# Optimization experiments

Measured on AMD Instinct MI355X. Metric: run time of the kernel, lower is better.

Reference implementation:

```python
import jax, jax.numpy as jnp
import numpy as np

N, L, D, H, DFF = 16, 192, 512, 8, 2048
HD = D // H


def _mha(q, k, v, wq, bq, wk, bk, wv, bv, wo, bo, mask=None):
    # q: [B, Lq, D], k/v: [B, Lk, D]
    B, Lq, _ = q.shape
    def proj(x, W, b):
        y = x @ W + b
        return y.reshape(B, -1, H, HD).transpose(0, 2, 1, 3)  # [B, H, L, HD]
    Q, K, V = proj(q, wq, bq), proj(k, wk, bk), proj(v, wv, bv)
    QK = jnp.einsum('bhqd,bhkd->bhqk', Q, K) / jnp.sqrt(jnp.asarray(HD, Q.dtype))
    if mask is not None:
        QK = QK + (1.0 - mask) * (-1e9)
    A = jax.nn.softmax(QK, axis=-1)
    out = jnp.einsum('bhqk,bhkd->bhqd', A, V).transpose(0, 2, 1, 3).reshape(B, Lq, D)
    return out @ wo + bo


def _ln(x, g, b, eps=1e-6):
    mu = x.mean(-1, keepdims=True)
    var = ((x - mu) ** 2).mean(-1, keepdims=True)
    return (x - mu) / jnp.sqrt(var + eps) * g + b


def setup_inputs() -> dict:
    key = jax.random.key(0)
    ks = jax.random.split(key, 16)
    w = lambda k, sh: jax.random.normal(k, sh, jnp.float32) * 0.02
    inp = {
        'S': jax.random.normal(ks[0], (N, L, D), jnp.float32),
        'padding_mask': jax.random.randint(ks[1], (N * N, 1, 1, L), 0, 2, dtype=jnp.int32),
        'training': 0,
    }
    for i, nm in enumerate(['ca_wq', 'ca_wk', 'ca_wv', 'ca_wo', 'ia_wq', 'ia_wk', 'ia_wv', 'ia_wo']):
        inp[nm] = w(ks[2 + i], (D, D))
        inp[nm.replace('w', 'b')] = jnp.zeros((D,), jnp.float32)
    inp['ffn_w1'] = w(ks[10], (D, DFF)); inp['ffn_b1'] = jnp.zeros((DFF,), jnp.float32)
    inp['ffn_w2'] = w(ks[11], (DFF, D)); inp['ffn_b2'] = jnp.zeros((D,), jnp.float32)
    inp['ln1_g'] = jnp.ones((D,), jnp.float32); inp['ln1_b'] = jnp.zeros((D,), jnp.float32)
    inp['ln2_g'] = jnp.ones((D,), jnp.float32); inp['ln2_b'] = jnp.zeros((D,), jnp.float32)
    return inp


def reference(S, ca_wq, ca_bq, ca_wk, ca_bk, ca_wv, ca_bv, ca_wo, ca_bo,
              ia_wq, ia_bq, ia_wk, ia_bk, ia_wv, ia_bv, ia_wo, ia_bo,
              ffn_w1, ffn_b1, ffn_w2, ffn_b2, ln1_g, ln1_b, ln2_g, ln2_b,
              padding_mask, training):
    # training == 0 -> dropout layers are identity (inference mode)
    mask = padding_mask.astype(S.dtype)
    n, l, d = S.shape
    # all-pairs cross attention: query seq i attends to key/value seq j
    queries = jnp.repeat(S, n, axis=0)   # [n*n, l, d]
    keyvalue = jnp.tile(S, (n, 1, 1))    # [n*n, l, d]
    S_attn = _mha(queries, keyvalue, keyvalue,
                  ca_wq, ca_bq, ca_wk, ca_bk, ca_wv, ca_bv, ca_wo, ca_bo, mask=mask)
    S_attn = S_attn.reshape(n, n, l, d).transpose(1, 2, 0, 3).reshape(n * l, n, d)
    S_flip = S.reshape(n * l, 1, d)
    S_attn = _mha(S_flip, S_attn, S_attn,
                  ia_wq, ia_bq, ia_wk, ia_bk, ia_wv, ia_bv, ia_wo, ia_bo)
    S_attn = S_attn.reshape(n, l, d)
    S_norm = _ln(S + S_attn, ln1_g, ln1_b)
    S_ffn = jax.nn.relu(S_norm @ ffn_w1 + ffn_b1) @ ffn_w2 + ffn_b2
    return _ln(S_norm + S_ffn, ln2_g, ln2_b)
```

## Files before the change

### kernel.cpp

```cpp
#include <hip/hip_runtime.h>


using u16 = unsigned short;
using u32 = unsigned int;
typedef __attribute__((ext_vector_type(8))) short short8;
typedef __attribute__((ext_vector_type(4))) float f32x4;

__device__ __forceinline__ u32 cvtpk(float lo, float hi) {
  u32 r;
  asm("v_cvt_pk_bf16_f32 %0, %1, %2" : "=v"(r) : "v"(lo), "v"(hi));
  return r;
}
__device__ __forceinline__ u16 f2bf(float f) { return (u16)cvtpk(f, f); }
__device__ __forceinline__ float bf2f(u16 h) {
  return __uint_as_float(((u32)h) << 16);
}
__device__ __forceinline__ f32x4 mfma16(short8 a, short8 b, f32x4 c) {
  return __builtin_amdgcn_mfma_f32_16x16x32_bf16(a, b, c, 0, 0, 0);
}
__device__ __forceinline__ void gload16(const void* g, u16* l) {
  __builtin_amdgcn_global_load_lds(
      (const __attribute__((address_space(1))) void*)g,
      (__attribute__((address_space(3))) void*)l, 16, 0, 0);
}

template<int ROWS, int NT>
__device__ __forceinline__ void stage_g16(u16* lds, const u16* __restrict__ src,
                                          int ld, int tid) {
  constexpr int UNITS = ROWS * 8;
  constexpr int WV = NT / 64;
  int lane = tid & 63, w = tid >> 6;
  #pragma unroll
  for (int u = 0; u < UNITS / NT; ++u) {
    int base = (u * WV + w) * 64;
    int unit = base + lane;
    int row = unit >> 3, co = unit & 7;
    gload16(src + (long)row * ld + ((co ^ (row & 7)) << 3), lds + base * 8);
  }
}
template<int ROWS, int NT>
__device__ __forceinline__ void stage_f32(u16* lds, const float* __restrict__ src,
                                          int ld, int tid) {
  constexpr int UNITS = ROWS * 8;
  #pragma unroll
  for (int u = 0; u < UNITS / NT; ++u) {
    int unit = tid + u * NT;
    int row = unit >> 3, co = unit & 7;
    const float* g = src + (long)row * ld + (co << 3);
    float4 a = *(const float4*)g;
    float4 b = *(const float4*)(g + 4);
    u32 p[4] = {cvtpk(a.x, a.y), cvtpk(a.z, a.w),
                cvtpk(b.x, b.y), cvtpk(b.z, b.w)};
    *(uint4*)&lds[(row << 6) + ((co ^ (row & 7)) << 3)] = *(const uint4*)p;
  }
}

template<typename AT, typename BT, int BM, int BN, int WM, int WN>
__device__ __forceinline__ void gemm_core(const AT* __restrict__ A, int lda,
                                          const BT* __restrict__ Bt, int ldb, int K,
                                          u16* As, u16* Bs,
                                          f32x4 (&acc)[BM / (WM * 16)][BN / (WN * 16)]) {
  constexpr int NT = WM * WN * 64;
  constexpr int MI = BM / (WM * 16), NJ = BN / (WN * 16);
  int tid = threadIdx.x, lane = tid & 63, wid = tid >> 6;
  int wr = wid % WM, wc = wid / WM;
  int g = lane >> 4, c = lane & 15;
  #pragma unroll
  for (int mi = 0; mi < MI; ++mi)
    #pragma unroll
    for (int nj = 0; nj < NJ; ++nj)
      acc[mi][nj] = f32x4{0.f, 0.f, 0.f, 0.f};
  for (int kb = 0; kb < K; kb += 64) {
    __syncthreads();
    if constexpr (sizeof(AT) == 4) stage_f32<BM, NT>(As, A + kb, lda, tid);
    else                           stage_g16<BM, NT>(As, A + kb, lda, tid);
    if constexpr (sizeof(BT) == 4) stage_f32<BN, NT>(Bs, Bt + kb, ldb, tid);
    else                           stage_g16<BN, NT>(Bs, Bt + kb, ldb, tid);
    __syncthreads();
    #pragma unroll
    for (int kk = 0; kk < 2; ++kk) {
      int sl = ((kk * 4 + g) ^ (c & 7)) << 3;
      short8 af[MI], bfr[NJ];
      #pragma unroll
      for (int mi = 0; mi < MI; ++mi)
        af[mi] = *(const short8*)&As[((wr * (BM / WM) + mi * 16 + c) << 6) + sl];
      #pragma unroll
      for (int nj = 0; nj < NJ; ++nj)
        bfr[nj] = *(const short8*)&Bs[((wc * (BN / WN) + nj * 16 + c) << 6) + sl];
      #pragma unroll
      for (int mi = 0; mi < MI; ++mi)
        #pragma unroll
        for (int nj = 0; nj < NJ; ++nj)
          acc[mi][nj] = mfma16(af[mi], bfr[nj], acc[mi][nj]);
    }
  }
}

__global__ __launch_bounds__(256) void k_cast(const float* __restrict__ S,
                                              u16* __restrict__ Sb) {
  int idx = (blockIdx.x * 256 + threadIdx.x) * 8;
  float4 a = *(const float4*)(S + idx);
  float4 b = *(const float4*)(S + idx + 4);
  u32 p[4] = {cvtpk(a.x, a.y), cvtpk(a.z, a.w),
              cvtpk(b.x, b.y), cvtpk(b.z, b.w)};
  *(uint4*)(Sb + idx) = *(const uint4*)p;
}

struct TJob { const float* src; u16* dst; int R, C, tile0; };
struct TJobs { TJob j[9]; };

__global__ __launch_bounds__(256) void k_transpose(TJobs jobs) {
  __shared__ float tile[32][33];
  int t = blockIdx.x;
  int ji = 0;
  #pragma unroll
  for (int k = 1; k < 9; ++k)
    if (t >= jobs.j[k].tile0) ji = k;
  TJob jb = jobs.j[ji];
  int lt = t - jb.tile0;
  int tpr = jb.C >> 5;
  int tr = lt / tpr, tc = lt % tpr;
  int tid = threadIdx.x;
  #pragma unroll
  for (int u = 0; u < 4; ++u) {
    int e = tid + u * 256;
    int r = e >> 5, cc = e & 31;
    tile[r][cc] = jb.src[(long)(tr * 32 + r) * jb.C + tc * 32 + cc];
  }
  __syncthreads();
  #pragma unroll
  for (int u = 0; u < 4; ++u) {
    int e = tid + u * 256;
    int r = e >> 5, cc = e & 31;
    jb.dst[(long)(tc * 32 + r) * jb.R + tr * 32 + cc] = f2bf(tile[cc][r]);
  }
}

__global__ __launch_bounds__(256) void k_qkv(const u16* __restrict__ Sb,
    const u16* __restrict__ btAll,
    const float* __restrict__ b0, const float* __restrict__ b1,
    const float* __restrict__ b2, const float* __restrict__ b3,
    u16* __restrict__ Qc, u16* __restrict__ Kc, u16* __restrict__ Vt,
    u16* __restrict__ Qi) {
  __shared__ u16 SH[16384];
  int f = blockIdx.x;
  int swz = (f & 7) * 48 + (f >> 3);
  int mb = swz >> 4, nb = swz & 15;
  f32x4 acc[4][4];
  gemm_core<u16, u16, 128, 128, 2, 2>(Sb + (long)mb * 128 * 512, 512,
                                      btAll + (long)nb * 128 * 512, 512, 512,
                                      SH, SH + 8192, acc);
  int z = nb >> 2;
  const float* bias = z == 0 ? b0 : z == 1 ? b1 : z == 2 ? b2 : b3;
  float scale = (z == 0 || z == 3) ? 0.125f : 1.0f;
  int lane = threadIdx.x & 63, wid = threadIdx.x >> 6;
  int wr = wid & 1, wc = wid >> 1, g = lane >> 4, cl = lane & 15;
  #pragma unroll
  for (int mi = 0; mi < 4; ++mi)
    #pragma unroll
    for (int nj = 0; nj < 4; ++nj)
      #pragma unroll
      for (int r = 0; r < 4; ++r) {
        int row = mb * 128 + wr * 64 + mi * 16 + g * 4 + r;
        int cz = (nb & 3) * 128 + wc * 64 + nj * 16 + cl;
        float v = (acc[mi][nj][r] + bias[cz]) * scale;
        int seq = row / 192, t = row % 192, h = cz >> 6, hd = cz & 63;
        if (z == 0)      Qc[((long)(seq * 8 + h) * 192 + t) * 64 + hd] = f2bf(v);
        else if (z == 1) Kc[((long)(seq * 8 + h) * 192 + t) * 64 + hd] = f2bf(v);
        else if (z == 2) Vt[((long)(seq * 8 + h) * 64 + hd) * 192 + t] = f2bf(v);
        else             Qi[(long)row * 512 + cz] = f2bf(v);
      }
}

__global__ __launch_bounds__(256) void k_attn_up(const u16* __restrict__ Qc,
    const u16* __restrict__ Kc, const u16* __restrict__ VtG,
    const int* __restrict__ mask, u16* __restrict__ AC,
    const u16* __restrict__ Qi, const float* __restrict__ wk,
    u16* __restrict__ U, int attnBlocks) {
  __shared__ __align__(16) u16 SH[24960];
  int bid = blockIdx.x;
  int tid = threadIdx.x, lane = tid & 63, w = tid >> 6;
  int g = lane >> 4, c = lane & 15;
  if (bid < attnBlocks) {
    u16* Ks = SH;
    u16* Vs = SH + 12288;
    float* mbf = (float*)(SH + 24576);
    int b = bid >> 3, h = bid & 7;
    int i = b >> 4, j = b & 15;
    int qb = w * 48;

    const u16* Kbase = Kc + (long)(j * 8 + h) * 192 * 64;
    #pragma unroll
    for (int u = 0; u < 6; ++u) {
      int base = (u * 4 + w) * 64;
      int unit = base + lane;
      int row = unit >> 3, co = unit & 7;
      gload16(Kbase + (long)row * 64 + ((co ^ (row & 7)) << 3), Ks + base * 8);
    }
    const u16* Vbase = VtG + (long)(j * 8 + h) * 64 * 192;
    #pragma unroll
    for (int u = 0; u < 6; ++u) {
      int base = (u * 4 + w) * 64;
      int unit = base + lane;
      int row = unit / 24, co = unit - row * 24;
      gload16(Vbase + (long)row * 192 + ((co ^ (row & 7)) << 3), Vs + base * 8);
    }
    short8 bq[3][2];
    const u16* Qbase = Qc + (long)(i * 8 + h) * 192 * 64;
    #pragma unroll
    for (int nj = 0; nj < 3; ++nj)
      #pragma unroll
      for (int ks = 0; ks < 2; ++ks)
        bq[nj][ks] = *(const short8*)(Qbase + (long)(qb + nj * 16 + c) * 64 + ks * 32 + g * 8);
    if (tid < 192) mbf[tid] = mask[(long)b * 192 + tid] ? 0.f : -1e9f;
    __syncthreads();

    f32x4 oa[4][3];
    #pragma unroll
    for (int mi = 0; mi < 4; ++mi)
      #pragma unroll
      for (int nj = 0; nj < 3; ++nj)
        oa[mi][nj] = f32x4{0.f, 0.f, 0.f, 0.f};
    float sm[3] = {0.f, 0.f, 0.f};
    int srcLo = c | ((g & 1) << 5);
    int srcHi = srcLo + 16;
    int hi = g & 2;

    #pragma unroll 2
    for (int s = 0; s < 6; ++s) {
      short8 ak[2][2];
      #pragma unroll
      for (int kh = 0; kh < 2; ++kh) {
        int row = (2 * s + kh) * 16 + c;
        #pragma unroll
        for (int ks = 0; ks < 2; ++ks)
          ak[kh][ks] = *(const short8*)&Ks[(row << 6) + (((ks * 4 + g) ^ (c & 7)) << 3)];
      }
      f32x4 sa[2][3];
      __builtin_amdgcn_s_setprio(1);
      #pragma unroll
      for (int kh = 0; kh < 2; ++kh)
        #pragma unroll
        for (int nj = 0; nj < 3; ++nj) {
          sa[kh][nj] = mfma16(ak[kh][0], bq[nj][0], f32x4{0.f, 0.f, 0.f, 0.f});
          sa[kh][nj] = mfma16(ak[kh][1], bq[nj][1], sa[kh][nj]);
        }
      __builtin_amdgcn_s_setprio(0);
      u32 pk[2][3][2];
      #pragma unroll
      for (int kh = 0; kh < 2; ++kh) {
        f32x4 m4 = *(const f32x4*)&mbf[(2 * s + kh) * 16 + g * 4];
        #pragma unroll
        for (int nj = 0; nj < 3; ++nj) {
          float p0 = __expf(sa[kh][nj][0] + m4[0]);
          float p1 = __expf(sa[kh][nj][1] + m4[1]);
          float p2 = __expf(sa[kh][nj][2] + m4[2]);
          float p3 = __expf(sa[kh][nj][3] + m4[3]);
          sm[nj] += (p0 + p1) + (p2 + p3);
          pk[kh][nj][0] = cvtpk(p0, p1);
          pk[kh][nj][1] = cvtpk(p2, p3);
        }
      }
      short8 bfg[3];
      #pragma unroll
      for (int nj = 0; nj < 3; ++nj) {
        u32 w0a = (u32)__shfl((int)pk[0][nj][0], srcLo);
        u32 w0b = (u32)__shfl((int)pk[1][nj][0], srcLo);
        u32 w1a = (u32)__shfl((int)pk[0][nj][1], srcLo);
        u32 w1b = (u32)__shfl((int)pk[1][nj][1], srcLo);
        u32 w2a = (u32)__shfl((int)pk[0][nj][0], srcHi);
        u32 w2b = (u32)__shfl((int)pk[1][nj][0], srcHi);
        u32 w3a = (u32)__shfl((int)pk[0][nj][1], srcHi);
        u32 w3b = (u32)__shfl((int)pk[1][nj][1], srcHi);
        union { u32 u[4]; short8 s8; } bf;
        bf.u[0] = hi ? w0b : w0a;
        bf.u[1] = hi ? w1b : w1a;
        bf.u[2] = hi ? w2b : w2a;
        bf.u[3] = hi ? w3b : w3a;
        bfg[nj] = bf.s8;
      }
      int sl = ((s * 4 + g) ^ (c & 7)) << 3;
      __builtin_amdgcn_s_setprio(1);
      #pragma unroll
      for (int mi = 0; mi < 4; ++mi) {
        short8 av = *(const short8*)&Vs[(mi * 16 + c) * 192 + sl];
        #pragma unroll
        for (int nj = 0; nj < 3; ++nj)
          oa[mi][nj] = mfma16(av, bfg[nj], oa[mi][nj]);
      }
      __builtin_amdgcn_s_setprio(0);
    }
    #pragma unroll
    for (int nj = 0; nj < 3; ++nj) {
      sm[nj] += __shfl_xor(sm[nj], 16);
      sm[nj] += __shfl_xor(sm[nj], 32);
    }
    #pragma unroll
    for (int nj = 0; nj < 3; ++nj) {
      float rs = 1.0f / sm[nj];
      int q = qb + nj * 16 + c;
      u16* dst = AC + ((long)(b * 192 + q)) * 512 + h * 64 + g * 4;
      #pragma unroll
      for (int mi = 0; mi < 4; ++mi) {
        u32 p2[2] = {cvtpk(oa[mi][nj][0] * rs, oa[mi][nj][1] * rs),
                     cvtpk(oa[mi][nj][2] * rs, oa[mi][nj][3] * rs)};
        *(uint2*)(dst + mi * 16) = *(const uint2*)p2;
      }
    }
  } else {
    u16* As = SH;
    u16* Bs = SH + 8192;
    int t = bid - attnBlocks;
    int mb = t % 24, r2 = t / 24;
    int nb = r2 & 3, h = r2 >> 2;
    f32x4 acc[4][4];
    gemm_core<u16, float, 128, 128, 2, 2>(Qi + (long)mb * 128 * 512 + h * 64, 512,
                                          wk + (long)nb * 128 * 512 + h * 64, 512, 64,
                                          As, Bs, acc);
    int wr = w & 1, wc = w >> 1, cl = lane & 15;
    #pragma unroll
    for (int mi = 0; mi < 4; ++mi)
      #pragma unroll
      for (int nj = 0; nj < 4; ++nj)
        #pragma unroll
        for (int r = 0; r < 4; ++r) {
          int row = mb * 128 + wr * 64 + mi * 16 + g * 4 + r;
          int col = nb * 128 + wc * 64 + nj * 16 + cl;
          U[((long)row * 8 + h) * 512 + col] = f2bf(acc[mi][nj][r]);
        }
  }
}

__global__ __launch_bounds__(512, 1) void k_oproj8(const u16* __restrict__ AC,
    const u16* __restrict__ woT, const float* __restrict__ bo,
    u16* __restrict__ S2) {
  extern __shared__ u16 LDS[];
  int f = blockIdx.x;
  int swz = (f & 7) * 48 + (f >> 3);
  int mb = swz >> 1, nb = swz & 1;
  int tid = threadIdx.x, lane = tid & 63, wid = tid >> 6;
  int wr = wid >> 2, wc = wid & 3;
  int g = lane >> 4, c = lane & 15;
  const u16* Abase = AC + (long)mb * 256 * 512;
  const u16* Bbase = woT + (long)nb * 256 * 512;

  auto STAGE = [&](int opOff, int buf, int half, int kt, const u16* base) {
    u16* ldst = LDS + opOff + buf * 16384 + half * 8192;
    const u16* gsrc = base + (long)half * 128 * 512 + kt * 64;
    #pragma unroll
    for (int u = 0; u < 2; ++u) {
      int unit = tid + u * 512;
      int row = unit >> 3, co = unit & 7;
      gload16(gsrc + (long)row * 512 + ((co ^ (row & 7)) << 3), ldst + unit * 8);
    }
  };

  f32x4 acc[8][4];
  #pragma unroll
  for (int mi = 0; mi < 8; ++mi)
    #pragma unroll
    for (int nj = 0; nj < 4; ++nj)
      acc[mi][nj] = f32x4{0.f, 0.f, 0.f, 0.f};

  STAGE(0, 0, 0, 0, Abase);     STAGE(0, 0, 1, 0, Abase);
  STAGE(32768, 0, 0, 0, Bbase); STAGE(32768, 0, 1, 0, Bbase);
  STAGE(0, 1, 0, 1, Abase);     STAGE(0, 1, 1, 1, Abase);
  STAGE(32768, 1, 0, 1, Bbase); STAGE(32768, 1, 1, 1, Bbase);
  asm volatile("s_waitcnt vmcnt(8)");
  __builtin_amdgcn_s_barrier();

  short8 aLo[8], aHi[8], bLo[4], bHi[4];
  for (int t = 0; t < 8; ++t) {
    int buf = t & 1;
    int abase = buf * 16384, bbase = 32768 + buf * 16384;
    #pragma unroll
    for (int m = 0; m < 4; ++m)
      #pragma unroll
      for (int kk = 0; kk < 2; ++kk)
        aLo[m * 2 + kk] = *(const short8*)&LDS[abase +
            (wr * 128 + m * 16 + c) * 64 + (((kk * 4 + g) ^ (c & 7)) << 3)];
    #pragma unroll
    for (int n = 0; n < 2; ++n)
      #pragma unroll
      for (int kk = 0; kk < 2; ++kk)
        bLo[n * 2 + kk] = *(const short8*)&LDS[bbase +
            (wc * 64 + n * 16 + c) * 64 + (((kk * 4 + g) ^ (c & 7)) << 3)];
    __builtin_amdgcn_s_barrier();
    asm volatile("s_waitcnt lgkmcnt(0)");
    __builtin_amdgcn_sched_barrier(0);
    __builtin_amdgcn_s_setprio(1);
    #pragma unroll
    for (int m = 0; m < 4; ++m)
      #pragma unroll
      for (int n = 0; n < 2; ++n)
        #pragma unroll
        for (int kk = 0; kk < 2; ++kk)
          acc[m][n] = mfma16(aLo[m * 2 + kk], bLo[n * 2 + kk], acc[m][n]);
    __builtin_amdgcn_s_setprio(0);
    __builtin_amdgcn_s_barrier();
    #pragma unroll
    for (int m = 0; m < 4; ++m)
      #pragma unroll
      for (int kk = 0; kk < 2; ++kk)
        aHi[m * 2 + kk] = *(const short8*)&LDS[abase +
            (wr * 128 + (4 + m) * 16 + c) * 64 + (((kk * 4 + g) ^ (c & 7)) << 3)];
    __builtin_amdgcn_s_barrier();
    asm volatile("s_waitcnt lgkmcnt(0)");
    __builtin_amdgcn_sched_barrier(0);
    __builtin_amdgcn_s_setprio(1);
    #pragma unroll
    for (int m = 0; m < 4; ++m)
      #pragma unroll
      for (int n = 0; n < 2; ++n)
        #pragma unroll
        for (int kk = 0; kk < 2; ++kk)
          acc[4 + m][n] = mfma16(aHi[m * 2 + kk], bLo[n * 2 + kk], acc[4 + m][n]);
    __builtin_amdgcn_s_setprio(0);
    __builtin_amdgcn_s_barrier();
    #pragma unroll
    for (int n = 0; n < 2; ++n)
      #pragma unroll
      for (int kk = 0; kk < 2; ++kk)
        bHi[n * 2 + kk] = *(const short8*)&LDS[bbase +
            (wc * 64 + (2 + n) * 16 + c) * 64 + (((kk * 4 + g) ^ (c & 7)) << 3)];
    if (t < 6) {
      STAGE(0, buf, 0, t + 2, Abase);
      STAGE(0, buf, 1, t + 2, Abase);
    }
    __builtin_amdgcn_s_barrier();
    asm volatile("s_waitcnt lgkmcnt(0)");
    __builtin_amdgcn_sched_barrier(0);
    __builtin_amdgcn_s_setprio(1);
    #pragma unroll
    for (int m = 0; m < 4; ++m)
      #pragma unroll
      for (int n = 0; n < 2; ++n)
        #pragma unroll
        for (int kk = 0; kk < 2; ++kk)
          acc[m][2 + n] = mfma16(aLo[m * 2 + kk], bHi[n * 2 + kk], acc[m][2 + n]);
    __builtin_amdgcn_s_setprio(0);
    __builtin_amdgcn_s_barrier();
    if (t < 6) {
      STAGE(32768, buf, 0, t + 2, Bbase);
      STAGE(32768, buf, 1, t + 2, Bbase);
    }
    __builtin_amdgcn_s_setprio(1);
    #pragma unroll
    for (int m = 0; m < 4; ++m)
      #pragma unroll
      for (int n = 0; n < 2; ++n)
        #pragma unroll
        for (int kk = 0; kk < 2; ++kk)
          acc[4 + m][2 + n] = mfma16(aHi[m * 2 + kk], bHi[n * 2 + kk], acc[4 + m][2 + n]);
    __builtin_amdgcn_s_setprio(0);
    if (t < 6)      asm volatile("s_waitcnt vmcnt(8)");
    else if (t == 6) asm volatile("s_waitcnt vmcnt(0)");
    if (t < 7) __builtin_amdgcn_s_barrier();
  }
  #pragma unroll
  for (int nj = 0; nj < 4; ++nj) {
    int col = nb * 256 + wc * 64 + nj * 16 + c;
    float bv = bo[col];
    #pragma unroll
    for (int mi = 0; mi < 8; ++mi)
      #pragma unroll
      for (int r = 0; r < 4; ++r) {
        int row = mb * 256 + wr * 128 + mi * 16 + g * 4 + r;
        S2[(long)row * 512 + col] = f2bf(acc[mi][nj][r] + bv);
      }
  }
}

__global__ __launch_bounds__(256) void k_ia_attn(const u16* __restrict__ S2,
    const u16* __restrict__ U, const u16* __restrict__ Qi,
    const float* __restrict__ bk, u16* __restrict__ Y) {
  __shared__ u16 s2[16 * 520];
  __shared__ float Lp[4][16][17];
  __shared__ float aL[8][16];
  __shared__ float cL[8];
  int tok = blockIdx.x;
  int tid = threadIdx.x, lane = tid & 63, w = tid >> 6;
  {
    const u16* src = S2 + (long)tok * 512;
    #pragma unroll
    for (int u = 0; u < 4; ++u) {
      int e = tid + u * 256;
      int r = e >> 6, cc = (e & 63) << 3;
      *(uint4*)&s2[r * 520 + cc] = *(const uint4*)(src + (long)r * 3072 * 512 + cc);
    }
  }
  if (w == 0) {
    int h = lane >> 3, p = lane & 7;
    short8 qv = *(const short8*)(Qi + (long)tok * 512 + h * 64 + p * 8);
    const float* bkp = bk + h * 64 + p * 8;
    float s = 0.f;
    #pragma unroll
    for (int v = 0; v < 8; ++v) s += bf2f((u16)qv[v]) * bkp[v];
    s += __shfl_xor(s, 1); s += __shfl_xor(s, 2); s += __shfl_xor(s, 4);
    if (p == 0) cL[h] = s;
  }
  __syncthreads();
  {
    int g = lane >> 4, c = lane & 15;
    const u16* Ub = U + (long)tok * 4096 + (long)(c & 7) * 512;
    f32x4 accL = {0.f, 0.f, 0.f, 0.f};
    #pragma unroll
    for (int kk = 0; kk < 4; ++kk) {
      int d = w * 128 + kk * 32 + g * 8;
      short8 aS = *(const short8*)&s2[c * 520 + d];
      short8 bU = *(const short8*)(Ub + d);
      accL = mfma16(aS, bU, accL);
    }
    #pragma unroll
    for (int r = 0; r < 4; ++r) Lp[w][g * 4 + r][c] = accL[r];
  }
  __syncthreads();
  if (w == 0) {
    int h = lane & 7, i0 = lane >> 3;
    float L0 = Lp[0][i0][h] + Lp[1][i0][h] + Lp[2][i0][h] + Lp[3][i0][h] + cL[h];
    float L1 = Lp[0][i0 + 8][h] + Lp[1][i0 + 8][h] + Lp[2][i0 + 8][h] +
               Lp[3][i0 + 8][h] + cL[h];
    float e0 = __expf(L0), e1 = __expf(L1);
    float s = e0 + e1;
    s += __shfl_xor(s, 8); s += __shfl_xor(s, 16); s += __shfl_xor(s, 32);
    float rs = 1.0f / s;
    aL[h][i0] = e0 * rs;
    aL[h][i0 + 8] = e1 * rs;
  }
  __syncthreads();
  {
    int h = tid & 7, d0 = (tid >> 3) << 4;
    float y[16];
    #pragma unroll
    for (int v = 0; v < 16; ++v) y[v] = 0.f;
    #pragma unroll
    for (int i = 0; i < 16; ++i) {
      float a = aL[h][i];
      short8 v0 = *(const short8*)&s2[i * 520 + d0];
      short8 v1 = *(const short8*)&s2[i * 520 + d0 + 8];
      #pragma unroll
      for (int v = 0; v < 8; ++v) {
        y[v]     += a * bf2f((u16)v0[v]);
        y[8 + v] += a * bf2f((u16)v1[v]);
      }
    }
    u32 o[8];
    #pragma unroll
    for (int v = 0; v < 8; ++v) o[v] = cvtpk(y[2 * v], y[2 * v + 1]);
    u16* dst = Y + ((long)tok * 8 + h) * 512 + d0;
    *(uint4*)dst = *(const uint4*)&o[0];
    *(uint4*)(dst + 8) = *(const uint4*)&o[4];
  }
}

__global__ __launch_bounds__(256) void k_vapply(const u16* __restrict__ Y,
    const u16* __restrict__ wvT, const float* __restrict__ bv,
    u16* __restrict__ AO) {
  __shared__ u16 As[128 * 64];
  __shared__ u16 Bs[64 * 64];
  int mb = blockIdx.x, h = blockIdx.z;
  f32x4 acc[2][4];
  gemm_core<u16, u16, 128, 64, 4, 1>(Y + (long)mb * 128 * 4096 + h * 512, 4096,
                                     wvT + (long)h * 64 * 512, 512, 512,
                                     As, Bs, acc);
  int lane = threadIdx.x & 63, wid = threadIdx.x >> 6;
  int g = lane >> 4, cl = lane & 15;
  #pragma unroll
  for (int mi = 0; mi < 2; ++mi)
    #pragma unroll
    for (int nj = 0; nj < 4; ++nj)
      #pragma unroll
      for (int r = 0; r < 4; ++r) {
        int row = mb * 128 + wid * 32 + mi * 16 + g * 4 + r;
        int col = h * 64 + nj * 16 + cl;
        AO[(long)row * 512 + col] = f2bf(acc[mi][nj][r] + bv[col]);
      }
}

__global__ __launch_bounds__(256) void k_gemm_f32out(const u16* __restrict__ A, int K,
    const u16* __restrict__ BT, const float* __restrict__ bias,
    float* __restrict__ out) {
  __shared__ u16 As[128 * 64];
  __shared__ u16 Bs[64 * 64];
  int f = blockIdx.x;
  int swz = (f & 7) * 24 + (f >> 3);
  int mb = swz >> 3, nb = swz & 7;
  f32x4 acc[4][2];
  gemm_core<u16, u16, 128, 64, 2, 2>(A + (long)mb * 128 * K, K,
                                     BT + (long)nb * 64 * K, K, K, As, Bs, acc);
  int lane = threadIdx.x & 63, wid = threadIdx.x >> 6;
  int wr = wid & 1, wc = wid >> 1, g = lane >> 4, cl = lane & 15;
  #pragma unroll
  for (int mi = 0; mi < 4; ++mi)
    #pragma unroll
    for (int nj = 0; nj < 2; ++nj)
      #pragma unroll
      for (int r = 0; r < 4; ++r) {
        int row = mb * 128 + wr * 64 + mi * 16 + g * 4 + r;
        int col = nb * 64 + wc * 32 + nj * 16 + cl;
        out[(long)row * 512 + col] = acc[mi][nj][r] + bias[col];
      }
}

__global__ __launch_bounds__(256) void k_ffn1(const u16* __restrict__ A,
    const u16* __restrict__ BT, const float* __restrict__ bias,
    u16* __restrict__ out) {
  __shared__ u16 As[128 * 64];
  __shared__ u16 Bs[128 * 64];
  int f = blockIdx.x;
  int swz = (f & 7) * 48 + (f >> 3);
  int mb = swz >> 4, nb = swz & 15;
  f32x4 acc[4][4];
  gemm_core<u16, u16, 128, 128, 2, 2>(A + (long)mb * 128 * 512, 512,
                                      BT + (long)nb * 128 * 512, 512, 512,
                                      As, Bs, acc);
  int lane = threadIdx.x & 63, wid = threadIdx.x >> 6;
  int wr = wid & 1, wc = wid >> 1, g = lane >> 4, cl = lane & 15;
  #pragma unroll
  for (int mi = 0; mi < 4; ++mi)
    #pragma unroll
    for (int nj = 0; nj < 4; ++nj)
      #pragma unroll
      for (int r = 0; r < 4; ++r) {
        int row = mb * 128 + wr * 64 + mi * 16 + g * 4 + r;
        int col = nb * 128 + wc * 64 + nj * 16 + cl;
        out[(long)row * 2048 + col] = f2bf(fmaxf(acc[mi][nj][r] + bias[col], 0.f));
      }
}

__global__ __launch_bounds__(256) void k_ln(const float* __restrict__ X1,
    const float* __restrict__ X2, const float* __restrict__ gg,
    const float* __restrict__ bb, float* __restrict__ outF,
    u16* __restrict__ outB) {
  __shared__ float red[8];
  int row = blockIdx.x, tid = threadIdx.x;
  long base = (long)row * 512;
  float x0 = X1[base + tid] + X2[base + tid];
  float x1 = X1[base + tid + 256] + X2[base + tid + 256];
  float s = x0 + x1, ss = x0 * x0 + x1 * x1;
  #pragma unroll
  for (int m = 1; m <= 32; m <<= 1) {
    s += __shfl_xor(s, m);
    ss += __shfl_xor(ss, m);
  }
  int w = tid >> 6;
  if ((tid & 63) == 0) { red[w] = s; red[4 + w] = ss; }
  __syncthreads();
  s = red[0] + red[1] + red[2] + red[3];
  ss = red[4] + red[5] + red[6] + red[7];
  float mu = s * (1.0f / 512.0f);
  float var = ss * (1.0f / 512.0f) - mu * mu;
  float rstd = 1.0f / sqrtf(var + 1e-6f);
  float y0 = (x0 - mu) * rstd * gg[tid] + bb[tid];
  float y1 = (x1 - mu) * rstd * gg[tid + 256] + bb[tid + 256];
  if (outF) { outF[base + tid] = y0; outF[base + tid + 256] = y1; }
  if (outB) { outB[base + tid] = f2bf(y0); outB[base + tid + 256] = f2bf(y1); }
}

extern "C" void kernel_launch(void* const* d_in, const int* in_sizes, int n_in,
                              void* d_out, int out_size, void* d_ws, size_t ws_size,
                              hipStream_t stream) {
  const float* S      = (const float*)d_in[0];
  const int*   maskp  = (const int*)d_in[1];
  const float* ca_wq  = (const float*)d_in[3];
  const float* ca_bq  = (const float*)d_in[4];
  const float* ca_wk  = (const float*)d_in[5];
  const float* ca_bk  = (const float*)d_in[6];
  const float* ca_wv  = (const float*)d_in[7];
  const float* ca_bv  = (const float*)d_in[8];
  const float* ca_wo  = (const float*)d_in[9];
  const float* ca_bo  = (const float*)d_in[10];
  const float* ia_wq  = (const float*)d_in[11];
  const float* ia_bq  = (const float*)d_in[12];
  const float* ia_wk  = (const float*)d_in[13];
  const float* ia_bk  = (const float*)d_in[14];
  const float* ia_wv  = (const float*)d_in[15];
  const float* ia_bv  = (const float*)d_in[16];
  const float* ia_wo  = (const float*)d_in[17];
  const float* ia_bo  = (const float*)d_in[18];
  const float* ffn_w1 = (const float*)d_in[19];
  const float* ffn_b1 = (const float*)d_in[20];
  const float* ffn_w2 = (const float*)d_in[21];
  const float* ffn_b2 = (const float*)d_in[22];
  const float* ln1_g  = (const float*)d_in[23];
  const float* ln1_b  = (const float*)d_in[24];
  const float* ln2_g  = (const float*)d_in[25];
  const float* ln2_b  = (const float*)d_in[26];

  char* ws = (char*)d_ws;
  constexpr size_t OFF_WQT  = 0;
  constexpr size_t OFF_WOTC = 2097152;
  constexpr size_t OFF_WVTI = 2621440;
  constexpr size_t OFF_WOTI = 3145728;
  constexpr size_t OFF_W1T  = 3670016;
  constexpr size_t OFF_W2T  = 5767168;
  constexpr size_t OFF_QC   = 7864320;
  constexpr size_t OFF_KC   = 11010048;
  constexpr size_t OFF_VT   = 14155776;
  constexpr size_t OFF_QI   = 17301504;
  constexpr size_t OFF_AC   = 20447232;
  constexpr size_t OFF_S2   = 70778880;
  constexpr size_t OFF_UBIG = 121110528;
  constexpr size_t NEED_BIG = OFF_UBIG + 25165824;
  constexpr size_t OFF_SB   = OFF_AC;
  constexpr size_t OFF_Y    = OFF_AC + 25165824;
  constexpr size_t OFF_AO   = OFF_QI;
  constexpr size_t OFF_IAO  = OFF_QC;
  constexpr size_t OFF_SNB  = OFF_VT;
  constexpr size_t OFF_SNF  = OFF_S2;
  constexpr size_t OFF_HFF  = OFF_S2 + 6291456;
  constexpr size_t OFF_FFO  = OFF_HFF + 12582912;

  u16* wqT  = (u16*)(ws + OFF_WQT);
  u16* woTc = (u16*)(ws + OFF_WOTC);
  u16* wvTi = (u16*)(ws + OFF_WVTI);
  u16* woTi = (u16*)(ws + OFF_WOTI);
  u16* w1T  = (u16*)(ws + OFF_W1T);
  u16* w2T  = (u16*)(ws + OFF_W2T);
  u16* Qc   = (u16*)(ws + OFF_QC);
  u16* Kc   = (u16*)(ws + OFF_KC);
  u16* Vt   = (u16*)(ws + OFF_VT);
  u16* Qi   = (u16*)(ws + OFF_QI);
  u16* AC   = (u16*)(ws + OFF_AC);
  u16* Sb   = (u16*)(ws + OFF_SB);
  u16* S2   = (u16*)(ws + OFF_S2);
  u16* Y    = (u16*)(ws + OFF_Y);
  u16* AO   = (u16*)(ws + OFF_AO);
  float* IAO = (float*)(ws + OFF_IAO);
  u16* SNB  = (u16*)(ws + OFF_SNB);
  float* SNF = (float*)(ws + OFF_SNF);
  u16* HFF  = (u16*)(ws + OFF_HFF);
  float* FFO = (float*)(ws + OFF_FFO);

  bool bigws = ws_size >= NEED_BIG;
  u16* U = bigws ? (u16*)(ws + OFF_UBIG) : (u16*)(ws + OFF_AC);

  static bool attrDone = false;
  if (!attrDone) {
    (void)hipFuncSetAttribute(reinterpret_cast<const void*>(&k_oproj8),
                              hipFuncAttributeMaxDynamicSharedMemorySize, 131072);
    attrDone = true;
  }

  TJobs tj;
  int t0 = 0;
  auto SET = [&](int k, const float* s, u16* d, int R, int C) {
    tj.j[k].src = s; tj.j[k].dst = d; tj.j[k].R = R; tj.j[k].C = C; tj.j[k].tile0 = t0;
    t0 += (R / 32) * (C / 32);
  };
  SET(0, ca_wq, wqT, 512, 512);
  SET(1, ca_wk, wqT + 262144, 512, 512);
  SET(2, ca_wv, wqT + 524288, 512, 512);
  SET(3, ia_wq, wqT + 786432, 512, 512);
  SET(4, ca_wo, woTc, 512, 512);
  SET(5, ia_wv, wvTi, 512, 512);
  SET(6, ia_wo, woTi, 512, 512);
  SET(7, ffn_w1, w1T, 512, 2048);
  SET(8, ffn_w2, w2T, 2048, 512);

  k_cast<<<dim3(768), 256, 0, stream>>>(S, Sb);
  k_transpose<<<dim3(t0), 256, 0, stream>>>(tj);
  k_qkv<<<dim3(384), 256, 0, stream>>>(Sb, wqT, ca_bq, ca_bk, ca_bv, ia_bq,
                                       Qc, Kc, Vt, Qi);
  if (bigws) {
    k_attn_up<<<dim3(2816), 256, 0, stream>>>(Qc, Kc, Vt, maskp, AC, Qi, ia_wk,
                                              U, 2048);
    k_oproj8<<<dim3(384), 512, 131072, stream>>>(AC, woTc, ca_bo, S2);
  } else {
    k_attn_up<<<dim3(2048), 256, 0, stream>>>(Qc, Kc, Vt, maskp, AC, Qi, ia_wk,
                                              U, 2048);
    k_oproj8<<<dim3(384), 512, 131072, stream>>>(AC, woTc, ca_bo, S2);
    k_attn_up<<<dim3(768), 256, 0, stream>>>(Qc, Kc, Vt, maskp, AC, Qi, ia_wk,
                                             U, 0);
  }
  k_ia_attn<<<dim3(3072), 256, 0, stream>>>(S2, U, Qi, ia_bk, Y);
  k_vapply<<<dim3(24, 1, 8), 256, 0, stream>>>(Y, wvTi, ia_bv, AO);
  k_gemm_f32out<<<dim3(192), 256, 0, stream>>>(AO, 512, woTi, ia_bo, IAO);
  k_ln<<<dim3(3072), 256, 0, stream>>>(S, IAO, ln1_g, ln1_b, SNF, SNB);
  k_ffn1<<<dim3(384), 256, 0, stream>>>(SNB, w1T, ffn_b1, HFF);
  k_gemm_f32out<<<dim3(192), 256, 0, stream>>>(HFF, 2048, w2T, ffn_b2, FFO);
  k_ln<<<dim3(3072), 256, 0, stream>>>(SNF, FFO, ln2_g, ln2_b, (float*)d_out, nullptr);
}
```

Measured before the change: 220.9 us.

## Read K/V directly from global in attention, use exp2 softmax, split U GEMM tiles

The cross-attention blocks no longer stage K and V into LDS. Each wave reads its K rows and V^T fragments straight from global memory, which relies on L1/L2 hits, and LDS use shrinks so more blocks can be resident. Softmax now uses the raw v_exp_f32 (exp2) instruction, with log2(e) folded into the Q scale in the QKV epilogue. The U projection GEMM switches to 128x64 tiles with twice as many blocks, and the kernel now takes dynamic shared memory. The risk is higher global-memory latency on K/V reads, with no LDS reuse and no swizzle.

```diff
diff --git a/kernel.cpp b/kernel.cpp
--- a/kernel.cpp
+++ b/kernel.cpp
@@ -14,6 +14,11 @@
 __device__ __forceinline__ u16 f2bf(float f) { return (u16)cvtpk(f, f); }
 __device__ __forceinline__ float bf2f(u16 h) {
   return __uint_as_float(((u32)h) << 16);
+}
+__device__ __forceinline__ float exp2a(float x) {
+  float r;
+  asm("v_exp_f32 %0, %1" : "=v"(r) : "v"(x));
+  return r;
 }
 __device__ __forceinline__ f32x4 mfma16(short8 a, short8 b, f32x4 c) {
   return __builtin_amdgcn_mfma_f32_16x16x32_bf16(a, b, c, 0, 0, 0);
@@ -152,7 +157,7 @@
                                       SH, SH + 8192, acc);
   int z = nb >> 2;
   const float* bias = z == 0 ? b0 : z == 1 ? b1 : z == 2 ? b2 : b3;
-  float scale = (z == 0 || z == 3) ? 0.125f : 1.0f;
+  float scale = z == 0 ? 0.18033688011112042f : (z == 3 ? 0.125f : 1.0f);
   int lane = threadIdx.x & 63, wid = threadIdx.x >> 6;
   int wr = wid & 1, wc = wid >> 1, g = lane >> 4, cl = lane & 15;
   #pragma unroll
@@ -177,36 +182,20 @@
     const int* __restrict__ mask, u16* __restrict__ AC,
     const u16* __restrict__ Qi, const float* __restrict__ wk,
     u16* __restrict__ U, int attnBlocks) {
-  __shared__ __align__(16) u16 SH[24960];
+  extern __shared__ __align__(16) u16 SH[];
   int bid = blockIdx.x;
   int tid = threadIdx.x, lane = tid & 63, w = tid >> 6;
   int g = lane >> 4, c = lane & 15;
   if (bid < attnBlocks) {
-    u16* Ks = SH;
-    u16* Vs = SH + 12288;
-    float* mbf = (float*)(SH + 24576);
+    float* mbf = (float*)SH;
     int b = bid >> 3, h = bid & 7;
     int i = b >> 4, j = b & 15;
     int qb = w * 48;
 
     const u16* Kbase = Kc + (long)(j * 8 + h) * 192 * 64;
-    #pragma unroll
-    for (int u = 0; u < 6; ++u) {
-      int base = (u * 4 + w) * 64;
-      int unit = base + lane;
-      int row = unit >> 3, co = unit & 7;
-      gload16(Kbase + (long)row * 64 + ((co ^ (row & 7)) << 3), Ks + base * 8);
-    }
     const u16* Vbase = VtG + (long)(j * 8 + h) * 64 * 192;
-    #pragma unroll
-    for (int u = 0; u < 6; ++u) {
-      int base = (u * 4 + w) * 64;
-      int unit = base + lane;
-      int row = unit / 24, co = unit - row * 24;
-      gload16(Vbase + (long)row * 192 + ((co ^ (row & 7)) << 3), Vs + base * 8);
-    }
+    const u16* Qbase = Qc + (long)(i * 8 + h) * 192 * 64;
     short8 bq[3][2];
-    const u16* Qbase = Qc + (long)(i * 8 + h) * 192 * 64;
     #pragma unroll
     for (int nj = 0; nj < 3; ++nj)
       #pragma unroll
@@ -226,15 +215,13 @@
     int srcHi = srcLo + 16;
     int hi = g & 2;
 
-    #pragma unroll 2
     for (int s = 0; s < 6; ++s) {
       short8 ak[2][2];
       #pragma unroll
       for (int kh = 0; kh < 2; ++kh) {
-        int row = (2 * s + kh) * 16 + c;
-        #pragma unroll
-        for (int ks = 0; ks < 2; ++ks)
-          ak[kh][ks] = *(const short8*)&Ks[(row << 6) + (((ks * 4 + g) ^ (c & 7)) << 3)];
+        const u16* kr = Kbase + (long)((2 * s + kh) * 16 + c) * 64 + g * 8;
+        ak[kh][0] = *(const short8*)kr;
+        ak[kh][1] = *(const short8*)(kr + 32);
       }
       f32x4 sa[2][3];
       __builtin_amdgcn_s_setprio(1);
@@ -252,10 +239,10 @@
         f32x4 m4 = *(const f32x4*)&mbf[(2 * s + kh) * 16 + g * 4];
         #pragma unroll
         for (int nj = 0; nj < 3; ++nj) {
-          float p0 = __expf(sa[kh][nj][0] + m4[0]);
-          float p1 = __expf(sa[kh][nj][1] + m4[1]);
-          float p2 = __expf(sa[kh][nj][2] + m4[2]);
-          float p3 = __expf(sa[kh][nj][3] + m4[3]);
+          float p0 = exp2a(sa[kh][nj][0] + m4[0]);
+          float p1 = exp2a(sa[kh][nj][1] + m4[1]);
+          float p2 = exp2a(sa[kh][nj][2] + m4[2]);
+          float p3 = exp2a(sa[kh][nj][3] + m4[3]);
           sm[nj] += (p0 + p1) + (p2 + p3);
           pk[kh][nj][0] = cvtpk(p0, p1);
           pk[kh][nj][1] = cvtpk(p2, p3);
@@ -279,11 +266,10 @@
         bf.u[3] = hi ? w3b : w3a;
         bfg[nj] = bf.s8;
       }
-      int sl = ((s * 4 + g) ^ (c & 7)) << 3;
       __builtin_amdgcn_s_setprio(1);
       #pragma unroll
       for (int mi = 0; mi < 4; ++mi) {
-        short8 av = *(const short8*)&Vs[(mi * 16 + c) * 192 + sl];
+        short8 av = *(const short8*)(Vbase + (long)(mi * 16 + c) * 192 + s * 32 + g * 8);
         #pragma unroll
         for (int nj = 0; nj < 3; ++nj)
           oa[mi][nj] = mfma16(av, bfg[nj], oa[mi][nj]);
@@ -312,20 +298,20 @@
     u16* Bs = SH + 8192;
     int t = bid - attnBlocks;
     int mb = t % 24, r2 = t / 24;
-    int nb = r2 & 3, h = r2 >> 2;
-    f32x4 acc[4][4];
-    gemm_core<u16, float, 128, 128, 2, 2>(Qi + (long)mb * 128 * 512 + h * 64, 512,
-                                          wk + (long)nb * 128 * 512 + h * 64, 512, 64,
-                                          As, Bs, acc);
+    int nb = r2 & 7, h = r2 >> 3;
+    f32x4 acc[4][2];
+    gemm_core<u16, float, 128, 64, 2, 2>(Qi + (long)mb * 128 * 512 + h * 64, 512,
+                                         wk + (long)nb * 64 * 512 + h * 64, 512, 64,
+                                         As, Bs, acc);
     int wr = w & 1, wc = w >> 1, cl = lane & 15;
     #pragma unroll
     for (int mi = 0; mi < 4; ++mi)
       #pragma unroll
-      for (int nj = 0; nj < 4; ++nj)
+      for (int nj = 0; nj < 2; ++nj)
         #pragma unroll
         for (int r = 0; r < 4; ++r) {
           int row = mb * 128 + wr * 64 + mi * 16 + g * 4 + r;
-          int col = nb * 128 + wc * 64 + nj * 16 + cl;
+          int col = nb * 64 + wc * 32 + nj * 16 + cl;
           U[((long)row * 8 + h) * 512 + col] = f2bf(acc[mi][nj][r]);
         }
   }
@@ -763,15 +749,15 @@
   k_qkv<<<dim3(384), 256, 0, stream>>>(Sb, wqT, ca_bq, ca_bk, ca_bv, ia_bq,
                                        Qc, Kc, Vt, Qi);
   if (bigws) {
-    k_attn_up<<<dim3(2816), 256, 0, stream>>>(Qc, Kc, Vt, maskp, AC, Qi, ia_wk,
-                                              U, 2048);
+    k_attn_up<<<dim3(3584), 256, 24576, stream>>>(Qc, Kc, Vt, maskp, AC, Qi,
+                                                  ia_wk, U, 2048);
     k_oproj8<<<dim3(384), 512, 131072, stream>>>(AC, woTc, ca_bo, S2);
   } else {
-    k_attn_up<<<dim3(2048), 256, 0, stream>>>(Qc, Kc, Vt, maskp, AC, Qi, ia_wk,
-                                              U, 2048);
+    k_attn_up<<<dim3(2048), 256, 24576, stream>>>(Qc, Kc, Vt, maskp, AC, Qi,
+                                                  ia_wk, U, 2048);
     k_oproj8<<<dim3(384), 512, 131072, stream>>>(AC, woTc, ca_bo, S2);
-    k_attn_up<<<dim3(768), 256, 0, stream>>>(Qc, Kc, Vt, maskp, AC, Qi, ia_wk,
-                                             U, 0);
+    k_attn_up<<<dim3(1536), 256, 24576, stream>>>(Qc, Kc, Vt, maskp, AC, Qi,
+                                                  ia_wk, U, 0);
   }
   k_ia_attn<<<dim3(3072), 256, 0, stream>>>(S2, U, Qi, ia_bk, Y);
   k_vapply<<<dim3(24, 1, 8), 256, 0, stream>>>(Y, wvTi, ia_bv, AO);
```

Measured after the change: 236.1 us. 6.9% more time.
